# Kernel optimization log

Measured on AMD Instinct MI355X. Metric: run time of the kernel, lower is better.

The kernel has to match this reference:

```python
import jax, jax.numpy as jnp
import numpy as np
from jax.scipy.special import logsumexp

NEG = -1e9  # surrogate for -inf (keeps masking arithmetic and grads NaN-free)
ABSTRACT_PEN = 0.5


def setup_inputs() -> dict:
    key = jax.random.key(0)
    ks = jax.random.split(key, 5)
    B, T, b = 32, 256, 16
    action_logps = jax.nn.log_softmax(jax.random.normal(ks[0], (B, T, b)), axis=-1)
    stop_logps = jax.nn.log_softmax(jax.random.normal(ks[1], (B, T + 1, b, 2)), axis=-1)
    start_logps = jax.nn.log_softmax(jax.random.normal(ks[2], (B, T + 1, b)), axis=-1)
    causal_pens = jax.random.uniform(ks[3], (B, T + 1, T + 1, b))
    lengths = jax.random.randint(ks[4], (B,), 1, T + 1)
    masks = (jnp.arange(T)[None, :] < lengths[:, None]).astype(jnp.float32)
    return {"action_logps": action_logps, "stop_logps": stop_logps,
            "start_logps": start_logps, "causal_pens": causal_pens,
            "masks": masks, "lengths": lengths}


def _cc_loss(action_logps, stop_logps, start_logps, causal_pens, masks, lengths):
    B, T, b = action_logps.shape
    start_logps = start_logps - ABSTRACT_PEN
    stop_logps = stop_logps[..., ::-1]  # STOP_IX == 0 -> flip so index 1 = stop

    a_ts = jnp.swapaxes(action_logps, 0, 1)            # [T,B,b]
    stop_ts = jnp.swapaxes(stop_logps[:, 1:], 0, 1)    # [T,B,b,2]  stop_logps[:, t+1]
    start_ts = jnp.swapaxes(start_logps[:, :T], 0, 1)  # [T,B,b]
    m_ts = jnp.swapaxes(masks, 0, 1)                   # [T,B]

    # ---- cc_fw: f[t] has shape [B,b,t,2]; pad segment-start axis to T ----
    f0 = jnp.full((B, b, T, 2), NEG).at[:, 0, 0, 1].set(0.0)

    def fw_step(f_prev, xs):
        a_t, stop_t, start_t, t = xs
        # continue current option: positions < t-1
        cont = f_prev[..., 0:1] + a_t[:, :, None, None] + stop_t[:, :, None, :]
        # start a new option at position t-1
        seg = logsumexp(f_prev[..., 1], axis=(1, 2))  # [B]
        new_seg = seg[:, None, None] + start_t[:, :, None] + a_t[:, :, None] + stop_t  # [B,b,2]
        idx = jnp.arange(T)[None, None, :, None]
        f_t = jnp.where(idx == t - 1, new_seg[:, :, None, :], cont)
        return f_t, f_t

    _, F = jax.lax.scan(fw_step, f0, (a_ts, stop_ts, start_ts, jnp.arange(1, T + 1)))
    F_full = jnp.concatenate([f0[None], F], axis=0)  # [T+1,B,b,T,2]
    total_logp = logsumexp(F_full[lengths, jnp.arange(B)][..., 1], axis=(1, 2))  # [B]

    # ---- cc_bw ----
    fT = jnp.full((B, b, 2), NEG).at[:, :, 1].set(0.0)

    def bw_step(f_next, xs):
        a_t, stop_t, start_t, m_t = xs
        f0c = a_t + logsumexp(stop_t + f_next, axis=2)  # [B,b]
        f1c = logsumexp(start_t[:, :, None] + a_t[:, :, None] + stop_t + f_next, axis=(1, 2))  # [B]
        f_t = jnp.stack([f0c, jnp.broadcast_to(f1c[:, None], f0c.shape)], axis=-1)
        done = jnp.stack([jnp.full_like(f0c, NEG), jnp.zeros_like(f0c)], axis=-1)
        f_t = jnp.where(m_t[:, None, None] > 0, f_t, done)
        return f_t, f_t

    _, BW = jax.lax.scan(bw_step, fT, (a_ts, stop_ts, start_ts, m_ts), reverse=True)
    BW_full = jnp.concatenate([BW, fT[None]], axis=0)  # [T+1,B,b,2]

    # ---- causal-consistency penalty expectation ----
    # marginal[t-1, B, b, start] = fw f[t][...,1] + bw f[t][...,1]
    marg = F[..., 1] + BW_full[1:][..., 1][:, :, :, None]          # [T,B,b,T]
    probs = jnp.exp(marg - total_logp[None, :, None, None])        # padded starts -> 0
    # pen[t-1, B, b, start] = causal_pens[B, start, t, b]
    pen = jnp.transpose(causal_pens[:, :T, 1:, :], (2, 0, 3, 1))   # [T,B,b,T]
    total_cc = jnp.sum(jnp.sum(probs * pen, axis=(2, 3)) * m_ts)
    return jnp.stack([jnp.sum(total_logp), total_cc])


def reference(action_logps, stop_logps, start_logps, causal_pens, masks, lengths):
    return _cc_loss(action_logps, stop_logps, start_logps, causal_pens, masks, lengths)
```

## Files before the change

kernel.cpp:

```cpp
#include <hip/hip_runtime.h>

constexpr int B  = 32;
constexpr int T  = 256;
constexpr int NB = 16;
#define INVLN2 1.4426950408889634f
#define LN2    0.6931471805599453f
#define AP2    (0.5f * 1.4426950408889634f)

__device__ __forceinline__ float fexp2(float x) { return exp2f(x); }
__device__ __forceinline__ float flog2(float x) { return __log2f(x); }

template<int C>
__device__ __forceinline__ float dppmv(float x) {
    return __int_as_float(__builtin_amdgcn_update_dpp(
        0, __float_as_int(x), C, 0xF, 0xF, true));
}

__device__ __forceinline__ float sum16(float x) {
    x += dppmv<0xB1>(x);
    x += dppmv<0x4E>(x);
    x += dppmv<0x141>(x);
    x += dppmv<0x140>(x);
    return x;
}

__global__ __launch_bounds__(256) void scan_kernel(
    const float* __restrict__ act_g,
    const float* __restrict__ stp_g,
    const float* __restrict__ str_g,
    const int*   __restrict__ len_g,
    float* __restrict__ Wbuf,
    float* __restrict__ TLbuf,
    float* __restrict__ Ubuf,
    float* __restrict__ Vbuf)
{
    __shared__ float sm[16384];
    float* act  = sm;
    float* stp  = sm + 4096;
    float* strt = sm + 4096 + 8192;

    const int beta = blockIdx.x;
    const int tid  = threadIdx.x;

    {
        const float4* a4 = (const float4*)(act_g + (size_t)beta * (T * NB));
        const float4* s4 = (const float4*)(stp_g + (size_t)beta * ((T + 1) * NB * 2) + 32);
        const float4* t4 = (const float4*)(str_g + (size_t)beta * ((T + 1) * NB));
        float4* actv = (float4*)act;
        float4* stpv = (float4*)stp;
        float4* strv = (float4*)strt;
        for (int i = tid; i < 1024; i += 256) {
            float4 v = a4[i];
            actv[i] = make_float4(v.x*INVLN2, v.y*INVLN2, v.z*INVLN2, v.w*INVLN2);
        }
        for (int i = tid; i < 2048; i += 256) {
            float4 v = s4[i];
            stpv[i] = make_float4(v.x*INVLN2, v.y*INVLN2, v.z*INVLN2, v.w*INVLN2);
        }
        for (int i = tid; i < 1024; i += 256) {
            float4 v = t4[i];
            strv[i] = make_float4(v.x*INVLN2, v.y*INVLN2, v.z*INVLN2, v.w*INVLN2);
        }
    }
    __syncthreads();

    const int wid  = tid >> 6;
    const int lane = tid & 63;
    const int b    = lane & 15;
    const int L    = len_g[beta];

    if (wid == 0) {
        float* Ub = Ubuf + (size_t)beta * (T * NB);
        float* Vb = Vbuf + (size_t)beta * ((T + 1) * NB);
        float PA = 0.f, Q = 0.f, Z = 0.f, TL = 0.f;
        float u0 = strt[b] - AP2;
        float E  = fexp2(u0);
        if (lane < 16) Ub[b] = u0;

        float  ca  = act[b];
        float2 cs  = *(const float2*)(stp + b * 2);
        float  cst = strt[16 + b];

        for (int t = 1; t <= T; ++t) {
            float  na  = act[(t & 255) * 16 + b];
            float2 ns  = *(const float2*)(stp + (t & 255) * 32 + b * 2);
            float  nst = strt[((t + 1) & 255) * 16 + b];

            float AP0 = fexp2(ca + cs.x);
            float S   = sum16(E * AP0);
            float G   = flog2(S) + Z;
            if (t == L) TL = G;
            float V   = PA + ca + Q + cs.x;
            PA += ca; Q += cs.y;
            if (lane < 16) Vb[t * 16 + b] = V;
            if (t < T) {
                float AP1 = fexp2(ca + cs.y);
                float Tb  = fexp2(cst - AP2);
                float U   = G + (cst - AP2) - PA - Q;
                if (lane < 16) Ub[t * 16 + b] = U;
                float En  = E * AP1 + S * Tb;
                unsigned e = (__float_as_uint(S) >> 23) & 0xFFu;
                float    r = __uint_as_float((254u - e) << 23);
                E = En * r;
                Z += (float)((int)e - 127);
            }
            ca = na; cs = ns; cst = nst;
        }
        if (lane == 0) TLbuf[beta] = TL;
    } else if (wid == 1) {
        float F0 = 0.f, F1 = 1.f, Z = 0.f;
        if (lane == 0) Wbuf[beta * (T + 1) + T] = 0.f;

        float  ca  = act[(T - 1) * 16 + b];
        float2 cs  = *(const float2*)(stp + (T - 1) * 32 + b * 2);
        float  cst = strt[(T - 1) * 16 + b];

        for (int i = T - 1; i >= 0; --i) {
            const int pr = (i - 1) & 255;
            float  na  = act[pr * 16 + b];
            float2 ns  = *(const float2*)(stp + pr * 32 + b * 2);
            float  nst = strt[pr * 16 + b];

            float AP1 = fexp2(ca + cs.y);
            float AP0 = fexp2(ca + cs.x);
            float Tb  = fexp2(cst - AP2);
            float F0n = AP1 * F0 + AP0 * F1;
            float F1n = sum16(Tb * F0n);
            const bool mk = (i < L);
            float W = flog2(F1n) + Z;
            unsigned e = (__float_as_uint(F1n) >> 23) & 0xFFu;
            float    r = __uint_as_float((254u - e) << 23);
            F0 = mk ? F0n * r : 0.f;
            F1 = mk ? F1n * r : 1.f;
            Z  = mk ? Z + (float)((int)e - 127) : 0.f;
            if (i >= 1 && lane == 0) Wbuf[beta * (T + 1) + i] = mk ? W : 0.f;
            ca = na; cs = ns; cst = nst;
        }
    }
}

__global__ __launch_bounds__(256) void cc_kernel(
    const float* __restrict__ pens,
    const int*   __restrict__ len_g,
    const float* __restrict__ Wbuf,
    const float* __restrict__ TLbuf,
    const float* __restrict__ Ubuf,
    const float* __restrict__ Vbuf,
    float* __restrict__ part)
{
    const int beta = blockIdx.x;
    const int t    = blockIdx.y + 1;
    const int tid  = threadIdx.x;
    const int pidx = blockIdx.y * B + beta;
    const int L    = len_g[beta];
    if (t > L) { if (tid == 0) part[pidx] = 0.f; return; }

    const float c0 = Wbuf[beta * (T + 1) + t] - TLbuf[beta];
    const float4* U4 = (const float4*)(Ubuf + (size_t)beta * (T * NB));
    const float4* P4 = (const float4*)(pens + (size_t)beta * ((size_t)(T+1)*(T+1)*NB)
                                            + (size_t)t * NB);
    const int q = tid & 3;
    float4 vq = ((const float4*)(Vbuf + (size_t)beta * ((T + 1) * NB) + t * NB))[q];
    vq.x += c0; vq.y += c0; vq.z += c0; vq.w += c0;

    float local = 0.f;
    const int n4 = t * 4;
    for (int i4 = tid; i4 < n4; i4 += 256) {
        const int tau = i4 >> 2;
        float4 u = U4[i4];
        float4 p = P4[(size_t)tau * ((T + 1) * 4) + (i4 & 3)];
        local += fexp2(u.x + vq.x) * p.x + fexp2(u.y + vq.y) * p.y
               + fexp2(u.z + vq.z) * p.z + fexp2(u.w + vq.w) * p.w;
    }
#pragma unroll
    for (int off = 1; off < 64; off <<= 1) local += __shfl_xor(local, off);
    __shared__ float red[4];
    if ((tid & 63) == 0) red[tid >> 6] = local;
    __syncthreads();
    if (tid == 0) part[pidx] = red[0] + red[1] + red[2] + red[3];
}

__global__ __launch_bounds__(256) void final_kernel(
    const float* __restrict__ part, const float* __restrict__ TLbuf,
    float* __restrict__ out)
{
    const int tid = threadIdx.x;
    const float4* p4 = (const float4*)part;
    float s = 0.f;
#pragma unroll
    for (int k = 0; k < 8; ++k) {
        float4 v = p4[tid + 256 * k];
        s += v.x + v.y + v.z + v.w;
    }
#pragma unroll
    for (int off = 1; off < 64; off <<= 1) s += __shfl_xor(s, off);
    __shared__ float red[4];
    if ((tid & 63) == 0) red[tid >> 6] = s;
    __syncthreads();
    if (tid == 0) out[1] = red[0] + red[1] + red[2] + red[3];

    float tl = (tid < 32) ? TLbuf[tid] : 0.f;
    if (tid < 64) {
#pragma unroll
        for (int off = 1; off < 32; off <<= 1) tl += __shfl_xor(tl, off);
        if (tid == 0) out[0] = tl * LN2;
    }
}

extern "C" void kernel_launch(void* const* d_in, const int* in_sizes, int n_in,
                              void* d_out, int out_size, void* d_ws, size_t ws_size,
                              hipStream_t stream) {
    (void)in_sizes; (void)n_in; (void)out_size; (void)ws_size;
    const float* act  = (const float*)d_in[0];
    const float* stp  = (const float*)d_in[1];
    const float* strt = (const float*)d_in[2];
    const float* pens = (const float*)d_in[3];
    const int*   lens = (const int*)d_in[5];
    float* out = (float*)d_out;

    float* ws    = (float*)d_ws;
    float* Wbuf  = ws;
    float* TLbuf = Wbuf + B * (T + 1);
    float* Ubuf  = TLbuf + B;
    float* Vbuf  = Ubuf + (size_t)B * T * NB;
    float* part  = Vbuf + (size_t)B * (T+1) * NB;

    scan_kernel<<<B, 256, 0, stream>>>(act, stp, strt, lens, Wbuf, TLbuf, Ubuf, Vbuf);
    cc_kernel<<<dim3(B, T), 256, 0, stream>>>(pens, lens, Wbuf, TLbuf, Ubuf, Vbuf, part);
    final_kernel<<<1, 256, 0, stream>>>(part, TLbuf, out);
}
```

Measured before the change: 261.6 us.

## Shorten serial scan critical path by precomputing exponentials and deferring logs

The per-step exp2 factors are now computed in parallel during the shared-memory load and stored as ready-to-use multipliers. The forward and backward scans only record (S, exponent) pairs, and the log2 calls and U/V outputs move to a parallel post-pass. A third wave builds prefix sums of act+stop with a segmented scan that feeds V/U. The goal is to strip transcendentals and global stores from the 256-step serial loops, which dominate scan latency. In exchange it adds two workspace buffers, an extra barrier phase and re-reads of global inputs.

```diff
diff --git a/kernel.cpp b/kernel.cpp
--- a/kernel.cpp
+++ b/kernel.cpp
@@ -32,35 +32,40 @@
     float* __restrict__ Wbuf,
     float* __restrict__ TLbuf,
     float* __restrict__ Ubuf,
-    float* __restrict__ Vbuf)
+    float* __restrict__ Vbuf,
+    float* __restrict__ SSbuf,
+    float* __restrict__ SBbuf)
 {
     __shared__ float sm[16384];
-    float* act  = sm;
-    float* stp  = sm + 4096;
-    float* strt = sm + 4096 + 8192;
+    float* A0 = sm;
+    float* A1 = sm + 4096;
+    float* TB = sm + 8192;
+    float* Cx = sm + 12288;
+    float* Gs = TB;
 
     const int beta = blockIdx.x;
     const int tid  = threadIdx.x;
 
-    {
-        const float4* a4 = (const float4*)(act_g + (size_t)beta * (T * NB));
-        const float4* s4 = (const float4*)(stp_g + (size_t)beta * ((T + 1) * NB * 2) + 32);
-        const float4* t4 = (const float4*)(str_g + (size_t)beta * ((T + 1) * NB));
-        float4* actv = (float4*)act;
-        float4* stpv = (float4*)stp;
-        float4* strv = (float4*)strt;
-        for (int i = tid; i < 1024; i += 256) {
-            float4 v = a4[i];
-            actv[i] = make_float4(v.x*INVLN2, v.y*INVLN2, v.z*INVLN2, v.w*INVLN2);
-        }
-        for (int i = tid; i < 2048; i += 256) {
-            float4 v = s4[i];
-            stpv[i] = make_float4(v.x*INVLN2, v.y*INVLN2, v.z*INVLN2, v.w*INVLN2);
-        }
-        for (int i = tid; i < 1024; i += 256) {
-            float4 v = t4[i];
-            strv[i] = make_float4(v.x*INVLN2, v.y*INVLN2, v.z*INVLN2, v.w*INVLN2);
-        }
+    const float4* a4 = (const float4*)(act_g + (size_t)beta * (T * NB));
+    const float4* s4 = (const float4*)(stp_g + (size_t)beta * ((T + 1) * NB * 2) + 32);
+    const float4* t4 = (const float4*)(str_g + (size_t)beta * ((T + 1) * NB));
+
+    for (int i4 = tid; i4 < 1024; i4 += 256) {
+        const int idx = i4 >> 2, q = i4 & 3;
+        float4 a  = a4[i4];
+        float4 sA = s4[idx * 8 + q * 2];
+        float4 sB = s4[idx * 8 + q * 2 + 1];
+        float4 st = t4[i4];
+        float4 v0, v1, vt;
+        v0.x = fexp2((a.x + sA.x) * INVLN2); v1.x = fexp2((a.x + sA.y) * INVLN2);
+        v0.y = fexp2((a.y + sA.z) * INVLN2); v1.y = fexp2((a.y + sA.w) * INVLN2);
+        v0.z = fexp2((a.z + sB.x) * INVLN2); v1.z = fexp2((a.z + sB.y) * INVLN2);
+        v0.w = fexp2((a.w + sB.z) * INVLN2); v1.w = fexp2((a.w + sB.w) * INVLN2);
+        vt.x = fexp2(st.x * INVLN2 - AP2); vt.y = fexp2(st.y * INVLN2 - AP2);
+        vt.z = fexp2(st.z * INVLN2 - AP2); vt.w = fexp2(st.w * INVLN2 - AP2);
+        ((float4*)A0)[i4] = v0;
+        ((float4*)A1)[i4] = v1;
+        ((float4*)TB)[i4] = vt;
     }
     __syncthreads();
 
@@ -70,72 +75,110 @@
     const int L    = len_g[beta];
 
     if (wid == 0) {
-        float* Ub = Ubuf + (size_t)beta * (T * NB);
-        float* Vb = Vbuf + (size_t)beta * ((T + 1) * NB);
-        float PA = 0.f, Q = 0.f, Z = 0.f, TL = 0.f;
-        float u0 = strt[b] - AP2;
-        float E  = fexp2(u0);
-        if (lane < 16) Ub[b] = u0;
-
-        float  ca  = act[b];
-        float2 cs  = *(const float2*)(stp + b * 2);
-        float  cst = strt[16 + b];
-
-        for (int t = 1; t <= T; ++t) {
-            float  na  = act[(t & 255) * 16 + b];
-            float2 ns  = *(const float2*)(stp + (t & 255) * 32 + b * 2);
-            float  nst = strt[((t + 1) & 255) * 16 + b];
-
-            float AP0 = fexp2(ca + cs.x);
-            float S   = sum16(E * AP0);
-            float G   = flog2(S) + Z;
-            if (t == L) TL = G;
-            float V   = PA + ca + Q + cs.x;
-            PA += ca; Q += cs.y;
-            if (lane < 16) Vb[t * 16 + b] = V;
-            if (t < T) {
-                float AP1 = fexp2(ca + cs.y);
-                float Tb  = fexp2(cst - AP2);
-                float U   = G + (cst - AP2) - PA - Q;
-                if (lane < 16) Ub[t * 16 + b] = U;
-                float En  = E * AP1 + S * Tb;
+        const float* A0b = A0 + b; const float* A1b = A1 + b; const float* TBb = TB + b;
+        float2* ss = (float2*)(SSbuf + beta * 512);
+        float E = TBb[0], Z = 0.f;
+        float a0c = A0b[0],  a1c = A1b[0],  tbc = TBb[16];
+        float a0n = A0b[16], a1n = A1b[16], tbn = TBb[32];
+        for (int idx = 0; idx < 256; ++idx) {
+            const int p = (idx + 2) & 255;
+            float a0p = A0b[p * 16], a1p = A1b[p * 16], tbp = TBb[((idx + 3) & 255) * 16];
+            float S = sum16(E * a0c);
+            if (lane == 0) ss[idx] = make_float2(S, Z);
+            if (idx < 255) {
+                float En = E * a1c + S * tbc;
                 unsigned e = (__float_as_uint(S) >> 23) & 0xFFu;
-                float    r = __uint_as_float((254u - e) << 23);
-                E = En * r;
+                E = En * __uint_as_float((254u - e) << 23);
                 Z += (float)((int)e - 127);
             }
-            ca = na; cs = ns; cst = nst;
-        }
-        if (lane == 0) TLbuf[beta] = TL;
+            a0c = a0n; a1c = a1n; tbc = tbn;
+            a0n = a0p; a1n = a1p; tbn = tbp;
+        }
     } else if (wid == 1) {
+        const float* A0b = A0 + b; const float* A1b = A1 + b; const float* TBb = TB + b;
+        float2* sb = (float2*)(SBbuf + beta * 512);
         float F0 = 0.f, F1 = 1.f, Z = 0.f;
-        if (lane == 0) Wbuf[beta * (T + 1) + T] = 0.f;
-
-        float  ca  = act[(T - 1) * 16 + b];
-        float2 cs  = *(const float2*)(stp + (T - 1) * 32 + b * 2);
-        float  cst = strt[(T - 1) * 16 + b];
-
-        for (int i = T - 1; i >= 0; --i) {
-            const int pr = (i - 1) & 255;
-            float  na  = act[pr * 16 + b];
-            float2 ns  = *(const float2*)(stp + pr * 32 + b * 2);
-            float  nst = strt[pr * 16 + b];
-
-            float AP1 = fexp2(ca + cs.y);
-            float AP0 = fexp2(ca + cs.x);
-            float Tb  = fexp2(cst - AP2);
-            float F0n = AP1 * F0 + AP0 * F1;
-            float F1n = sum16(Tb * F0n);
+        float a0c = A0b[255 * 16], a1c = A1b[255 * 16], tbc = TBb[255 * 16];
+        float a0n = A0b[254 * 16], a1n = A1b[254 * 16], tbn = TBb[254 * 16];
+        for (int i = 255; i >= 0; --i) {
+            const int p = (i - 2) & 255;
+            float a0p = A0b[p * 16], a1p = A1b[p * 16], tbp = TBb[p * 16];
+            float F0n = a1c * F0 + a0c * F1;
+            float F1n = sum16(tbc * F0n);
+            if (lane == 0) sb[i] = make_float2(F1n, Z);
             const bool mk = (i < L);
-            float W = flog2(F1n) + Z;
             unsigned e = (__float_as_uint(F1n) >> 23) & 0xFFu;
             float    r = __uint_as_float((254u - e) << 23);
             F0 = mk ? F0n * r : 0.f;
             F1 = mk ? F1n * r : 1.f;
             Z  = mk ? Z + (float)((int)e - 127) : 0.f;
-            if (i >= 1 && lane == 0) Wbuf[beta * (T + 1) + i] = mk ? W : 0.f;
-            ca = na; cs = ns; cst = nst;
-        }
+            a0c = a0n; a1c = a1n; tbc = tbn;
+            a0n = a0p; a1n = a1p; tbn = tbp;
+        }
+    } else if (wid == 2) {
+        const int seg = lane >> 4;
+        const float* ap = act_g + (size_t)beta * 4096 + b;
+        const float* sp = stp_g + (size_t)beta * 8224 + 32 + b * 2 + 1;
+        float s = 0.f;
+#pragma unroll 8
+        for (int k = 0; k < 64; ++k) {
+            const int idx = seg * 64 + k;
+            s += (ap[idx * 16] + sp[idx * 32]) * INVLN2;
+        }
+        float inc = s;
+        float u1 = __shfl_up(inc, 16); if (lane >= 16) inc += u1;
+        float u2 = __shfl_up(inc, 32); if (lane >= 32) inc += u2;
+        float run = inc - s;
+#pragma unroll 8
+        for (int k = 0; k < 64; ++k) {
+            const int idx = seg * 64 + k;
+            run += (ap[idx * 16] + sp[idx * 32]) * INVLN2;
+            Cx[idx * 16 + b] = run;
+        }
+    }
+    __syncthreads();
+
+    {
+        float2 sz = ((const float2*)(SSbuf + beta * 512))[tid];
+        float G = flog2(sz.x) + sz.y;
+        Gs[tid + 1] = G;
+        if (tid == L - 1) TLbuf[beta] = G;
+        if (tid >= 1) {
+            float2 fz = ((const float2*)(SBbuf + beta * 512))[tid];
+            Wbuf[beta * (T + 1) + tid] = (tid < L) ? flog2(fz.x) + fz.y : 0.f;
+        } else {
+            Wbuf[beta * (T + 1) + T] = 0.f;
+        }
+    }
+    __syncthreads();
+
+    float4* Ub4 = (float4*)(Ubuf + (size_t)beta * (T * NB));
+    float4* Vb4 = (float4*)(Vbuf + (size_t)beta * ((T + 1) * NB));
+    for (int i4 = tid; i4 < 1024; i4 += 256) {
+        const int row = i4 >> 2, q = i4 & 3;
+        float4 c  = ((const float4*)Cx)[i4];
+        float4 sA = s4[row * 8 + q * 2];
+        float4 sB = s4[row * 8 + q * 2 + 1];
+        float4 V;
+        V.x = c.x + (sA.x - sA.y) * INVLN2;
+        V.y = c.y + (sA.z - sA.w) * INVLN2;
+        V.z = c.z + (sB.x - sB.y) * INVLN2;
+        V.w = c.w + (sB.z - sB.w) * INVLN2;
+        Vb4[(row + 1) * 4 + q] = V;
+        float4 st = t4[i4];
+        float4 U;
+        if (row == 0) {
+            U.x = st.x * INVLN2 - AP2; U.y = st.y * INVLN2 - AP2;
+            U.z = st.z * INVLN2 - AP2; U.w = st.w * INVLN2 - AP2;
+        } else {
+            float g = Gs[row];
+            float4 cm = ((const float4*)Cx)[i4 - 4];
+            U.x = g + st.x * INVLN2 - AP2 - cm.x;
+            U.y = g + st.y * INVLN2 - AP2 - cm.y;
+            U.z = g + st.z * INVLN2 - AP2 - cm.z;
+            U.w = g + st.w * INVLN2 - AP2 - cm.w;
+        }
+        Ub4[i4] = U;
     }
 }
 
@@ -224,8 +267,10 @@
     float* Ubuf  = TLbuf + B;
     float* Vbuf  = Ubuf + (size_t)B * T * NB;
     float* part  = Vbuf + (size_t)B * (T+1) * NB;
-
-    scan_kernel<<<B, 256, 0, stream>>>(act, stp, strt, lens, Wbuf, TLbuf, Ubuf, Vbuf);
+    float* SSbuf = part + T * B;
+    float* SBbuf = SSbuf + B * 512;
+
+    scan_kernel<<<B, 256, 0, stream>>>(act, stp, strt, lens, Wbuf, TLbuf, Ubuf, Vbuf, SSbuf, SBbuf);
     cc_kernel<<<dim3(B, T), 256, 0, stream>>>(pens, lens, Wbuf, TLbuf, Ubuf, Vbuf, part);
     final_kernel<<<1, 256, 0, stream>>>(part, TLbuf, out);
 }
```

New measurement: 230.2 us. 12.0% less time.
